# Kernel tuning notes

Hardware: AMD Instinct MI355X
Metric: run time of the kernel (lower is better)

The kernel has to match this reference:

```python
import jax, jax.numpy as jnp
import numpy as np

B = 4096
IN_DIMS = (3, 32, 32)      # in_numel = 3072
OUT_DIMS = (64, 16, 16)    # out_numel = 16384
IN_NUMEL = int(np.prod(IN_DIMS))
OUT_NUMEL = int(np.prod(OUT_DIMS))


def setup_inputs() -> dict:
    key = jax.random.key(0)
    k1, k2, k3, k4 = jax.random.split(key, 4)
    x = jax.random.normal(k1, (B,) + IN_DIMS, dtype=jnp.float32)
    # Cached composed linear operator (out_numel x in_numel); scale ~1/sqrt(fan_in)
    cached_matrix = jax.random.normal(k2, (OUT_NUMEL, IN_NUMEL), dtype=jnp.float32) / np.sqrt(IN_NUMEL)
    cached_matrix_extra = jax.random.uniform(k3, (1,), dtype=jnp.float32) + 0.5
    cached_tensor_extra = jax.random.normal(k4, (IN_NUMEL, IN_NUMEL), dtype=jnp.float32) / IN_NUMEL
    return {
        "x": x,
        "cached_matrix": cached_matrix,
        "cached_matrix_extra": cached_matrix_extra,
        "cached_tensor_extra": cached_tensor_extra,
    }


def reference(x, cached_matrix, cached_matrix_extra, cached_tensor_extra):
    batches = x.shape[0]
    # input_as_matrix: [in_numel, B]
    X = x.reshape(batches, -1).T
    # input_as_matrix_extra: L2 norm per column -> [1, B]
    X_extra = jnp.linalg.norm(X, ord=2, axis=0, keepdims=True)
    # output_as_matrix = M @ X : [out_numel, B]
    Y = jnp.matmul(cached_matrix, X)
    # output_as_matrix_extra = s * ||x|| + sum((T @ X) * X, axis=0)
    Y_extra = cached_matrix_extra * X_extra + jnp.sum(jnp.matmul(cached_tensor_extra, X) * X, axis=0, keepdims=True)
    Y = Y / Y_extra
    return Y.T.reshape(batches, *OUT_DIMS)
```

## Files before the change

kernel.cpp:

```cpp
#include <hip/hip_runtime.h>
#include <hip/hip_bf16.h>

typedef __attribute__((ext_vector_type(8))) short bf16x8;
typedef __attribute__((ext_vector_type(4))) short bf16x4;
typedef __attribute__((ext_vector_type(4))) float f32x4;

#define DEV __device__ __forceinline__

static constexpr int BATCH = 4096;
static constexpr int KDIM  = 3072;
static constexpr int NOUT  = 16384;

DEV unsigned short f2bf(float f) {
  union { float f; unsigned int u; } v; v.f = f;
  unsigned int u = v.u;
  u += 0x7fffu + ((u >> 16) & 1u);
  return (unsigned short)(u >> 16);
}

__global__ __launch_bounds__(256) void prep_x_kernel(
    const float* __restrict__ x, unsigned short* __restrict__ xbf,
    float* __restrict__ nrm) {
  const int b = blockIdx.x;
  const int t = threadIdx.x;
  const float* row = x + (size_t)b * KDIM;
  unsigned short* orow = xbf + (size_t)b * KDIM;
  float ss = 0.f;
#pragma unroll
  for (int i = 0; i < 3; ++i) {
    const int c = i * 256 + t;
    float4 v = reinterpret_cast<const float4*>(row)[c];
    ss += v.x * v.x + v.y * v.y + v.z * v.z + v.w * v.w;
    bf16x4 o;
    o[0] = (short)f2bf(v.x); o[1] = (short)f2bf(v.y);
    o[2] = (short)f2bf(v.z); o[3] = (short)f2bf(v.w);
    reinterpret_cast<bf16x4*>(orow)[c] = o;
  }
#pragma unroll
  for (int off = 32; off > 0; off >>= 1) ss += __shfl_down(ss, off, 64);
  __shared__ float red[4];
  if ((t & 63) == 0) red[t >> 6] = ss;
  __syncthreads();
  if (t == 0) nrm[b] = sqrtf(red[0] + red[1] + red[2] + red[3]);
}

__global__ __launch_bounds__(256) void cvt_kernel(
    const float* __restrict__ src, unsigned short* __restrict__ dst, size_t n4) {
  size_t i = (size_t)blockIdx.x * blockDim.x + threadIdx.x;
  const size_t stride = (size_t)gridDim.x * blockDim.x;
  for (; i < n4; i += stride) {
    float4 v = reinterpret_cast<const float4*>(src)[i];
    bf16x4 o;
    o[0] = (short)f2bf(v.x); o[1] = (short)f2bf(v.y);
    o[2] = (short)f2bf(v.z); o[3] = (short)f2bf(v.w);
    reinterpret_cast<bf16x4*>(dst)[i] = o;
  }
}

__global__ __launch_bounds__(256) void qform_kernel(
    const unsigned short* __restrict__ A,
    const unsigned short* __restrict__ Bm,
    const float* __restrict__ xf,
    float* __restrict__ partial) {
  __shared__ unsigned short ldsA[128 * 32];
  __shared__ unsigned short ldsB[128 * 32];
  const int t = threadIdx.x;
  const int lane = t & 63;
  const int wv = t >> 6;
  const int wr = wv >> 1, wc = wv & 1;
  const int col0 = blockIdx.x * 128;
  const int row0 = blockIdx.y * 128;

  f32x4 acc[4][4];
#pragma unroll
  for (int i = 0; i < 4; ++i)
#pragma unroll
    for (int j = 0; j < 4; ++j) acc[i][j] = (f32x4){0.f, 0.f, 0.f, 0.f};

  const unsigned short* aBase = A + (size_t)row0 * KDIM;
  const unsigned short* bBase = Bm + (size_t)col0 * KDIM;
  const int ldsoff0 = (t & ~63) * 8;

  for (int k0 = 0; k0 < KDIM; k0 += 32) {
    __syncthreads();
#pragma unroll
    for (int i = 0; i < 2; ++i) {
      const int c = i * 256 + t;
      const unsigned short* ga = aBase + (size_t)(c >> 2) * KDIM + (k0 + (c & 3) * 8);
      const unsigned short* gb = bBase + (size_t)(c >> 2) * KDIM + (k0 + (c & 3) * 8);
      __builtin_amdgcn_global_load_lds(
          (const __attribute__((address_space(1))) unsigned int*)(const void*)ga,
          (__attribute__((address_space(3))) unsigned int*)(void*)(ldsA + i * 2048 + ldsoff0),
          16, 0, 0);
      __builtin_amdgcn_global_load_lds(
          (const __attribute__((address_space(1))) unsigned int*)(const void*)gb,
          (__attribute__((address_space(3))) unsigned int*)(void*)(ldsB + i * 2048 + ldsoff0),
          16, 0, 0);
    }
    __syncthreads();
    bf16x8 af[4], bfr[4];
#pragma unroll
    for (int mi = 0; mi < 4; ++mi)
      af[mi] = *reinterpret_cast<const bf16x8*>(
          &ldsA[(wr * 64 + mi * 16 + (lane & 15)) * 32 + (lane >> 4) * 8]);
#pragma unroll
    for (int ni = 0; ni < 4; ++ni)
      bfr[ni] = *reinterpret_cast<const bf16x8*>(
          &ldsB[(wc * 64 + ni * 16 + (lane & 15)) * 32 + (lane >> 4) * 8]);
#pragma unroll
    for (int mi = 0; mi < 4; ++mi)
#pragma unroll
      for (int ni = 0; ni < 4; ++ni)
        acc[mi][ni] = __builtin_amdgcn_mfma_f32_16x16x32_bf16(af[mi], bfr[ni], acc[mi][ni], 0, 0, 0);
  }

#pragma unroll
  for (int mi = 0; mi < 4; ++mi) {
#pragma unroll
    for (int j = 0; j < 4; ++j) {
      const int b = row0 + wr * 64 + mi * 16 + (lane >> 4) * 4 + j;
      const float* xrow = xf + (size_t)b * KDIM + col0 + wc * 64 + (lane & 15);
      float s = 0.f;
#pragma unroll
      for (int ni = 0; ni < 4; ++ni) s += acc[mi][ni][j] * xrow[ni * 16];
      s += __shfl_xor(s, 1, 64);
      s += __shfl_xor(s, 2, 64);
      s += __shfl_xor(s, 4, 64);
      s += __shfl_xor(s, 8, 64);
      if ((lane & 15) == 0) partial[(size_t)b * 48 + blockIdx.x * 2 + wc] = s;
    }
  }
}

__global__ __launch_bounds__(256) void finalize_ye_kernel(
    const float* __restrict__ nrm, const float* __restrict__ partial,
    const float* __restrict__ sp, float* __restrict__ ye) {
  const int b = blockIdx.x * blockDim.x + threadIdx.x;
  if (b >= BATCH) return;
  float qv = 0.f;
#pragma unroll
  for (int i = 0; i < 48; ++i) qv += partial[(size_t)b * 48 + i];
  ye[b] = sp[0] * nrm[b] + qv;
}

static constexpr int BK8 = 64;

#define LDSE(BUF, OP, HALF) ((BUF)*32768 + (OP)*16384 + (HALF)*8192)

#define STAGE8(OP, HALF, S, BUF)                                             \
  {                                                                          \
    const unsigned short* gb_ = (OP) ? Bm : A;                               \
    const int gr0_ = ((OP) ? col0 : row0) + (HALF)*128;                      \
    _Pragma("unroll")                                                        \
    for (int j_ = 0; j_ < 2; ++j_) {                                         \
      const int row_ = j_*64 + wid*8 + (lane >> 3);                          \
      const int le_  = ((lane & 7)*8) ^ ((row_ & 7) << 3);                   \
      __builtin_amdgcn_global_load_lds(                                      \
        (const __attribute__((address_space(1))) unsigned int*)(const void*) \
          (gb_ + (size_t)(gr0_ + row_)*KDIM + (S)*BK8 + le_),                \
        (__attribute__((address_space(3))) unsigned int*)(void*)             \
          (lds + LDSE(BUF, OP, HALF) + j_*4096 + wid*512),                   \
        16, 0, 0);                                                           \
    }                                                                        \
  }

#define LOADA8(P, QM)                                                        \
  _Pragma("unroll")                                                          \
  for (int mi = 0; mi < 4; ++mi) {                                           \
    const int r_ = wm*64 + mi*16 + (lane & 15);                              \
    const int xv_ = (r_ & 7) << 3;                                           \
    _Pragma("unroll")                                                        \
    for (int ks = 0; ks < 2; ++ks)                                           \
      aft[mi][ks] = *reinterpret_cast<const bf16x8*>(                        \
          lds + LDSE(P, 0, QM) + ((r_*64 + ks*32 + (lane >> 4)*8) ^ xv_));   \
  }

#define LOADB8(P, QN, DST)                                                   \
  _Pragma("unroll")                                                          \
  for (int ni = 0; ni < 2; ++ni) {                                           \
    const int r_ = wn*32 + ni*16 + (lane & 15);                              \
    const int xv_ = (r_ & 7) << 3;                                           \
    _Pragma("unroll")                                                        \
    for (int ks = 0; ks < 2; ++ks)                                           \
      DST[ni][ks] = *reinterpret_cast<const bf16x8*>(                        \
          lds + LDSE(P, 1, QN) + ((r_*64 + ks*32 + (lane >> 4)*8) ^ xv_));   \
  }

#define MMA8(QM, QN, BSRC)                                                   \
  __builtin_amdgcn_s_setprio(1);                                             \
  _Pragma("unroll")                                                          \
  for (int mi = 0; mi < 4; ++mi)                                             \
    _Pragma("unroll")                                                        \
    for (int ni = 0; ni < 2; ++ni)                                           \
      _Pragma("unroll")                                                      \
      for (int ks = 0; ks < 2; ++ks)                                         \
        acc[(QM)*4 + mi][(QN)*2 + ni] =                                      \
            __builtin_amdgcn_mfma_f32_16x16x32_bf16(                         \
                aft[mi][ks], BSRC[ni][ks], acc[(QM)*4 + mi][(QN)*2 + ni],    \
                0, 0, 0);                                                    \
  __builtin_amdgcn_s_setprio(0);

#define VMW(N)                                                               \
  asm volatile("s_waitcnt vmcnt(" #N ")" ::: "memory");                      \
  __builtin_amdgcn_sched_barrier(0)

#define BARR __builtin_amdgcn_s_barrier()

#define TILE8(P, T)                                                          \
  LOADA8(P, 0); LOADB8(P, 0, bft0);                                          \
  STAGE8(1, 1, (T)+1, (P)^1);                                                \
  BARR; MMA8(0, 0, bft0); BARR;                                              \
  LOADB8(P, 1, bft1);                                                        \
  STAGE8(1, 0, (T)+1, (P)^1);                                                \
  BARR; MMA8(0, 1, bft1); BARR;                                              \
  LOADA8(P, 1);                                                              \
  STAGE8(0, 0, (T)+2, P);                                                    \
  BARR; MMA8(1, 1, bft1); BARR;                                              \
  STAGE8(0, 1, (T)+2, P);                                                    \
  BARR; MMA8(1, 0, bft0); VMW(4); BARR;

__global__ __launch_bounds__(512) void gemm8_kernel(
    const unsigned short* __restrict__ A,
    const unsigned short* __restrict__ Bm,
    const float* __restrict__ ye,
    float* __restrict__ out) {
  __shared__ unsigned short lds[65536];
  const int t = threadIdx.x;
  const int lane = t & 63, wid = t >> 6;
  const int wm = wid >> 2, wn = wid & 3;

  const int bid = blockIdx.x;
  const int wgid = (bid & 7) * 128 + (bid >> 3);
  const int bx = wgid & 63;
  const int by = wgid >> 6;
  const int row0 = by * 256, col0 = bx * 256;

  f32x4 acc[8][4];
#pragma unroll
  for (int i = 0; i < 8; ++i)
#pragma unroll
    for (int j = 0; j < 4; ++j) acc[i][j] = (f32x4){0.f, 0.f, 0.f, 0.f};

  bf16x8 aft[4][2], bft0[2][2], bft1[2][2];

  STAGE8(0, 0, 0, 0); STAGE8(1, 0, 0, 0); STAGE8(0, 1, 0, 0); STAGE8(1, 1, 0, 0);
  STAGE8(0, 0, 1, 1); STAGE8(0, 1, 1, 1);
  VMW(4);
  BARR;

#pragma unroll 1
  for (int i = 0; i < 23; ++i) {
    const int t0 = 2 * i;
    TILE8(0, t0);
    TILE8(1, t0 + 1);
  }

  LOADA8(0, 0); LOADB8(0, 0, bft0);
  STAGE8(1, 1, 47, 1);
  BARR; MMA8(0, 0, bft0); BARR;
  LOADB8(0, 1, bft1);
  STAGE8(1, 0, 47, 1);
  BARR; MMA8(0, 1, bft1); BARR;
  LOADA8(0, 1);
  BARR; MMA8(1, 1, bft1); BARR;
  MMA8(1, 0, bft0); VMW(0); BARR;
  LOADA8(1, 0); LOADB8(1, 0, bft0);
  BARR; MMA8(0, 0, bft0); BARR;
  LOADB8(1, 1, bft1);
  BARR; MMA8(0, 1, bft1); BARR;
  LOADA8(1, 1);
  BARR; MMA8(1, 1, bft1); BARR;
  MMA8(1, 0, bft0);

#pragma unroll
  for (int am = 0; am < 8; ++am) {
#pragma unroll
    for (int j = 0; j < 4; ++j) {
      const int b = row0 + (am >> 2) * 128 + wm * 64 + (am & 3) * 16 +
                    (lane >> 4) * 4 + j;
      const float r = 1.0f / ye[b];
      float* orow = out + (size_t)b * NOUT + col0;
#pragma unroll
      for (int an = 0; an < 4; ++an)
        orow[(an >> 1) * 128 + wn * 32 + (an & 1) * 16 + (lane & 15)] =
            acc[am][an][j] * r;
    }
  }
}

__global__ __launch_bounds__(256) void main_gemm_kernel(
    const unsigned short* __restrict__ A,
    const float* __restrict__ Bf,
    const float* __restrict__ ye,
    float* __restrict__ out) {
  __shared__ unsigned short ldsA[128 * 32];
  __shared__ unsigned short ldsB[128 * 32];
  const int t = threadIdx.x;
  const int lane = t & 63;
  const int wv = t >> 6;
  const int wr = wv >> 1, wc = wv & 1;
  const int col0 = blockIdx.x * 128;
  const int row0 = blockIdx.y * 128;

  f32x4 acc[4][4];
#pragma unroll
  for (int i = 0; i < 4; ++i)
#pragma unroll
    for (int j = 0; j < 4; ++j) acc[i][j] = (f32x4){0.f, 0.f, 0.f, 0.f};

  const unsigned short* aBase = A + (size_t)row0 * KDIM;
  const float* bfBase = Bf + (size_t)col0 * KDIM;
  const int ldsoff0 = (t & ~63) * 8;

  for (int k0 = 0; k0 < KDIM; k0 += 32) {
    __syncthreads();
#pragma unroll
    for (int i = 0; i < 2; ++i) {
      const int c = i * 256 + t;
      const unsigned short* ga = aBase + (size_t)(c >> 2) * KDIM + (k0 + (c & 3) * 8);
      __builtin_amdgcn_global_load_lds(
          (const __attribute__((address_space(1))) unsigned int*)(const void*)ga,
          (__attribute__((address_space(3))) unsigned int*)(void*)(ldsA + i * 2048 + ldsoff0),
          16, 0, 0);
    }
#pragma unroll
    for (int i = 0; i < 2; ++i) {
      const int c = i * 256 + t;
      const int r = c >> 1, ko = (c & 1) * 16;
      const float* gp = bfBase + (size_t)r * KDIM + k0 + ko;
      unsigned short tmp[16];
#pragma unroll
      for (int q = 0; q < 4; ++q) {
        float4 v = reinterpret_cast<const float4*>(gp)[q];
        tmp[q * 4 + 0] = f2bf(v.x); tmp[q * 4 + 1] = f2bf(v.y);
        tmp[q * 4 + 2] = f2bf(v.z); tmp[q * 4 + 3] = f2bf(v.w);
      }
#pragma unroll
      for (int q = 0; q < 2; ++q)
        *reinterpret_cast<bf16x8*>(&ldsB[r * 32 + ko + q * 8]) =
            *reinterpret_cast<const bf16x8*>(&tmp[q * 8]);
    }
    __syncthreads();
    bf16x8 af[4], bfr[4];
#pragma unroll
    for (int mi = 0; mi < 4; ++mi)
      af[mi] = *reinterpret_cast<const bf16x8*>(
          &ldsA[(wr * 64 + mi * 16 + (lane & 15)) * 32 + (lane >> 4) * 8]);
#pragma unroll
    for (int ni = 0; ni < 4; ++ni)
      bfr[ni] = *reinterpret_cast<const bf16x8*>(
          &ldsB[(wc * 64 + ni * 16 + (lane & 15)) * 32 + (lane >> 4) * 8]);
#pragma unroll
    for (int mi = 0; mi < 4; ++mi)
#pragma unroll
      for (int ni = 0; ni < 4; ++ni)
        acc[mi][ni] = __builtin_amdgcn_mfma_f32_16x16x32_bf16(af[mi], bfr[ni], acc[mi][ni], 0, 0, 0);
  }

#pragma unroll
  for (int mi = 0; mi < 4; ++mi) {
#pragma unroll
    for (int j = 0; j < 4; ++j) {
      const int b = row0 + wr * 64 + mi * 16 + (lane >> 4) * 4 + j;
      const float r = 1.0f / ye[b];
      float* orow = out + (size_t)b * NOUT + col0 + wc * 64 + (lane & 15);
#pragma unroll
      for (int ni = 0; ni < 4; ++ni) orow[ni * 16] = acc[mi][ni][j] * r;
    }
  }
}

extern "C" void kernel_launch(void* const* d_in, const int* in_sizes, int n_in,
                              void* d_out, int out_size, void* d_ws, size_t ws_size,
                              hipStream_t stream) {
  (void)in_sizes; (void)n_in; (void)out_size;
  const float* x  = (const float*)d_in[0];
  const float* M  = (const float*)d_in[1];
  const float* sc = (const float*)d_in[2];
  const float* T  = (const float*)d_in[3];
  float* out = (float*)d_out;
  char* ws = (char*)d_ws;

  size_t off = 0;
  auto wsalloc = [&](size_t bytes) -> void* {
    void* p = ws + off;
    off += (bytes + 255) & ~(size_t)255;
    return p;
  };
  unsigned short* Xbf = (unsigned short*)wsalloc((size_t)BATCH * KDIM * 2);
  unsigned short* Tbf = (unsigned short*)wsalloc((size_t)KDIM * KDIM * 2);
  float* nrm = (float*)wsalloc((size_t)BATCH * 4);
  float* ye  = (float*)wsalloc((size_t)BATCH * 4);
  float* partial = (float*)wsalloc((size_t)BATCH * 48 * 4);
  unsigned short* Mbf = (unsigned short*)wsalloc((size_t)NOUT * KDIM * 2);
  const bool useMbf = (off <= ws_size);

  prep_x_kernel<<<BATCH, 256, 0, stream>>>(x, Xbf, nrm);
  cvt_kernel<<<1024, 256, 0, stream>>>(T, Tbf, (size_t)KDIM * KDIM / 4);
  if (useMbf)
    cvt_kernel<<<2048, 256, 0, stream>>>(M, Mbf, (size_t)NOUT * KDIM / 4);
  qform_kernel<<<dim3(KDIM / 128, BATCH / 128), 256, 0, stream>>>(Xbf, Tbf, x, partial);
  finalize_ye_kernel<<<BATCH / 256, 256, 0, stream>>>(nrm, partial, sc, ye);
  if (useMbf)
    gemm8_kernel<<<dim3((NOUT / 256) * (BATCH / 256)), 512, 0, stream>>>(
        Xbf, Mbf, ye, out);
  else
    main_gemm_kernel<<<dim3(NOUT / 128, BATCH / 128), 256, 0, stream>>>(
        Xbf, M, ye, out);
}
```

Baseline: 566.8 us.

## Port quadratic-form GEMM to pipelined 256x256 split-K kernel and remap tiles

Replaces the simple 128x128 quadratic-form GEMM (T @ X, then a dot product with X) with a version of the pipelined 256x256 MFMA kernel, split four ways over K to fill the GPU. The epilogue dots the accumulators with bf16 X and reduces through LDS into the partial buffer. It also remaps the main GEMM's block-to-tile assignment per XCD and adds an lgkmcnt wait before the first MMA stage. The main risk is lower precision in the quadratic form, since it now uses bf16 X instead of fp32.

New measurement: 560.9 us. Within noise of the previous version (-1.0%).

```diff
diff --git a/kernel.cpp b/kernel.cpp
--- a/kernel.cpp
+++ b/kernel.cpp
@@ -16,6 +16,12 @@
   unsigned int u = v.u;
   u += 0x7fffu + ((u >> 16) & 1u);
   return (unsigned short)(u >> 16);
+}
+
+DEV float bf2f(unsigned short h) {
+  union { unsigned int u; float f; } v;
+  v.u = ((unsigned int)h) << 16;
+  return v.f;
 }
 
 __global__ __launch_bounds__(256) void prep_x_kernel(
@@ -54,81 +60,6 @@
     o[0] = (short)f2bf(v.x); o[1] = (short)f2bf(v.y);
     o[2] = (short)f2bf(v.z); o[3] = (short)f2bf(v.w);
     reinterpret_cast<bf16x4*>(dst)[i] = o;
-  }
-}
-
-__global__ __launch_bounds__(256) void qform_kernel(
-    const unsigned short* __restrict__ A,
-    const unsigned short* __restrict__ Bm,
-    const float* __restrict__ xf,
-    float* __restrict__ partial) {
-  __shared__ unsigned short ldsA[128 * 32];
-  __shared__ unsigned short ldsB[128 * 32];
-  const int t = threadIdx.x;
-  const int lane = t & 63;
-  const int wv = t >> 6;
-  const int wr = wv >> 1, wc = wv & 1;
-  const int col0 = blockIdx.x * 128;
-  const int row0 = blockIdx.y * 128;
-
-  f32x4 acc[4][4];
-#pragma unroll
-  for (int i = 0; i < 4; ++i)
-#pragma unroll
-    for (int j = 0; j < 4; ++j) acc[i][j] = (f32x4){0.f, 0.f, 0.f, 0.f};
-
-  const unsigned short* aBase = A + (size_t)row0 * KDIM;
-  const unsigned short* bBase = Bm + (size_t)col0 * KDIM;
-  const int ldsoff0 = (t & ~63) * 8;
-
-  for (int k0 = 0; k0 < KDIM; k0 += 32) {
-    __syncthreads();
-#pragma unroll
-    for (int i = 0; i < 2; ++i) {
-      const int c = i * 256 + t;
-      const unsigned short* ga = aBase + (size_t)(c >> 2) * KDIM + (k0 + (c & 3) * 8);
-      const unsigned short* gb = bBase + (size_t)(c >> 2) * KDIM + (k0 + (c & 3) * 8);
-      __builtin_amdgcn_global_load_lds(
-          (const __attribute__((address_space(1))) unsigned int*)(const void*)ga,
-          (__attribute__((address_space(3))) unsigned int*)(void*)(ldsA + i * 2048 + ldsoff0),
-          16, 0, 0);
-      __builtin_amdgcn_global_load_lds(
-          (const __attribute__((address_space(1))) unsigned int*)(const void*)gb,
-          (__attribute__((address_space(3))) unsigned int*)(void*)(ldsB + i * 2048 + ldsoff0),
-          16, 0, 0);
-    }
-    __syncthreads();
-    bf16x8 af[4], bfr[4];
-#pragma unroll
-    for (int mi = 0; mi < 4; ++mi)
-      af[mi] = *reinterpret_cast<const bf16x8*>(
-          &ldsA[(wr * 64 + mi * 16 + (lane & 15)) * 32 + (lane >> 4) * 8]);
-#pragma unroll
-    for (int ni = 0; ni < 4; ++ni)
-      bfr[ni] = *reinterpret_cast<const bf16x8*>(
-          &ldsB[(wc * 64 + ni * 16 + (lane & 15)) * 32 + (lane >> 4) * 8]);
-#pragma unroll
-    for (int mi = 0; mi < 4; ++mi)
-#pragma unroll
-      for (int ni = 0; ni < 4; ++ni)
-        acc[mi][ni] = __builtin_amdgcn_mfma_f32_16x16x32_bf16(af[mi], bfr[ni], acc[mi][ni], 0, 0, 0);
-  }
-
-#pragma unroll
-  for (int mi = 0; mi < 4; ++mi) {
-#pragma unroll
-    for (int j = 0; j < 4; ++j) {
-      const int b = row0 + wr * 64 + mi * 16 + (lane >> 4) * 4 + j;
-      const float* xrow = xf + (size_t)b * KDIM + col0 + wc * 64 + (lane & 15);
-      float s = 0.f;
-#pragma unroll
-      for (int ni = 0; ni < 4; ++ni) s += acc[mi][ni][j] * xrow[ni * 16];
-      s += __shfl_xor(s, 1, 64);
-      s += __shfl_xor(s, 2, 64);
-      s += __shfl_xor(s, 4, 64);
-      s += __shfl_xor(s, 8, 64);
-      if ((lane & 15) == 0) partial[(size_t)b * 48 + blockIdx.x * 2 + wc] = s;
-    }
   }
 }
 
@@ -204,11 +135,14 @@
   asm volatile("s_waitcnt vmcnt(" #N ")" ::: "memory");                      \
   __builtin_amdgcn_sched_barrier(0)
 
+#define LGKMW8 asm volatile("s_waitcnt lgkmcnt(8)" ::: "memory")
+
 #define BARR __builtin_amdgcn_s_barrier()
 
 #define TILE8(P, T)                                                          \
   LOADA8(P, 0); LOADB8(P, 0, bft0);                                          \
   STAGE8(1, 1, (T)+1, (P)^1);                                                \
+  LGKMW8;                                                                    \
   BARR; MMA8(0, 0, bft0); BARR;                                              \
   LOADB8(P, 1, bft1);                                                        \
   STAGE8(1, 0, (T)+1, (P)^1);                                                \
@@ -219,6 +153,31 @@
   STAGE8(0, 1, (T)+2, P);                                                    \
   BARR; MMA8(1, 0, bft0); VMW(4); BARR;
 
+#define PROLOG8(T0)                                                          \
+  STAGE8(0, 0, (T0), 0); STAGE8(1, 0, (T0), 0);                              \
+  STAGE8(0, 1, (T0), 0); STAGE8(1, 1, (T0), 0);                              \
+  STAGE8(0, 0, (T0)+1, 1); STAGE8(0, 1, (T0)+1, 1);                          \
+  VMW(4);                                                                    \
+  BARR;
+
+#define TAIL8(TE)                                                            \
+  LOADA8(0, 0); LOADB8(0, 0, bft0);                                          \
+  STAGE8(1, 1, (TE)+1, 1);                                                   \
+  BARR; MMA8(0, 0, bft0); BARR;                                              \
+  LOADB8(0, 1, bft1);                                                        \
+  STAGE8(1, 0, (TE)+1, 1);                                                   \
+  BARR; MMA8(0, 1, bft1); BARR;                                              \
+  LOADA8(0, 1);                                                              \
+  BARR; MMA8(1, 1, bft1); BARR;                                              \
+  MMA8(1, 0, bft0); VMW(0); BARR;                                            \
+  LOADA8(1, 0); LOADB8(1, 0, bft0);                                          \
+  BARR; MMA8(0, 0, bft0); BARR;                                              \
+  LOADB8(1, 1, bft1);                                                        \
+  BARR; MMA8(0, 1, bft1); BARR;                                              \
+  LOADA8(1, 1);                                                              \
+  BARR; MMA8(1, 1, bft1); BARR;                                              \
+  MMA8(1, 0, bft0);
+
 __global__ __launch_bounds__(512) void gemm8_kernel(
     const unsigned short* __restrict__ A,
     const unsigned short* __restrict__ Bm,
@@ -230,9 +189,9 @@
   const int wm = wid >> 2, wn = wid & 3;
 
   const int bid = blockIdx.x;
-  const int wgid = (bid & 7) * 128 + (bid >> 3);
-  const int bx = wgid & 63;
-  const int by = wgid >> 6;
+  const int xcd = bid & 7, r = bid >> 3;
+  const int by = r >> 3;
+  const int bx = xcd * 8 + (r & 7);
   const int row0 = by * 256, col0 = bx * 256;
 
   f32x4 acc[8][4];
@@ -243,34 +202,14 @@
 
   bf16x8 aft[4][2], bft0[2][2], bft1[2][2];
 
-  STAGE8(0, 0, 0, 0); STAGE8(1, 0, 0, 0); STAGE8(0, 1, 0, 0); STAGE8(1, 1, 0, 0);
-  STAGE8(0, 0, 1, 1); STAGE8(0, 1, 1, 1);
-  VMW(4);
-  BARR;
-
+  PROLOG8(0);
 #pragma unroll 1
   for (int i = 0; i < 23; ++i) {
     const int t0 = 2 * i;
     TILE8(0, t0);
     TILE8(1, t0 + 1);
   }
-
-  LOADA8(0, 0); LOADB8(0, 0, bft0);
-  STAGE8(1, 1, 47, 1);
-  BARR; MMA8(0, 0, bft0); BARR;
-  LOADB8(0, 1, bft1);
-  STAGE8(1, 0, 47, 1);
-  BARR; MMA8(0, 1, bft1); BARR;
-  LOADA8(0, 1);
-  BARR; MMA8(1, 1, bft1); BARR;
-  MMA8(1, 0, bft0); VMW(0); BARR;
-  LOADA8(1, 0); LOADB8(1, 0, bft0);
-  BARR; MMA8(0, 0, bft0); BARR;
-  LOADB8(1, 1, bft1);
-  BARR; MMA8(0, 1, bft1); BARR;
-  LOADA8(1, 1);
-  BARR; MMA8(1, 1, bft1); BARR;
-  MMA8(1, 0, bft0);
+  TAIL8(46);
 
 #pragma unroll
   for (int am = 0; am < 8; ++am) {
@@ -278,13 +217,82 @@
     for (int j = 0; j < 4; ++j) {
       const int b = row0 + (am >> 2) * 128 + wm * 64 + (am & 3) * 16 +
                     (lane >> 4) * 4 + j;
-      const float r = 1.0f / ye[b];
+      const float rr = 1.0f / ye[b];
       float* orow = out + (size_t)b * NOUT + col0;
 #pragma unroll
       for (int an = 0; an < 4; ++an)
         orow[(an >> 1) * 128 + wn * 32 + (an & 1) * 16 + (lane & 15)] =
-            acc[am][an][j] * r;
+            acc[am][an][j] * rr;
     }
+  }
+}
+
+__global__ __launch_bounds__(512) void qform8_kernel(
+    const unsigned short* __restrict__ A,
+    const unsigned short* __restrict__ Bm,
+    float* __restrict__ partial) {
+  __shared__ unsigned short lds[65536];
+  const int t = threadIdx.x;
+  const int lane = t & 63, wid = t >> 6;
+  const int wm = wid >> 2, wn = wid & 3;
+
+  const int bid = blockIdx.x;
+  const int wgid = (bid & 7) * 96 + (bid >> 3);
+  const int jt = wgid / 64;
+  const int rem = wgid % 64;
+  const int bt = rem >> 2;
+  const int ks4 = rem & 3;
+  const int row0 = bt * 256, col0 = jt * 256;
+  const int k0t = ks4 * 12;
+
+  f32x4 acc[8][4];
+#pragma unroll
+  for (int i = 0; i < 8; ++i)
+#pragma unroll
+    for (int j = 0; j < 4; ++j) acc[i][j] = (f32x4){0.f, 0.f, 0.f, 0.f};
+
+  bf16x8 aft[4][2], bft0[2][2], bft1[2][2];
+
+  PROLOG8(k0t);
+#pragma unroll 1
+  for (int i = 0; i < 5; ++i) {
+    const int t0 = k0t + 2 * i;
+    TILE8(0, t0);
+    TILE8(1, t0 + 1);
+  }
+  TAIL8(k0t + 10);
+
+  float* sred = reinterpret_cast<float*>(lds);
+#pragma unroll
+  for (int am = 0; am < 8; ++am) {
+#pragma unroll
+    for (int j = 0; j < 4; ++j) {
+      const int b = row0 + (am >> 2) * 128 + wm * 64 + (am & 3) * 16 +
+                    (lane >> 4) * 4 + j;
+      float s = 0.f;
+#pragma unroll
+      for (int an = 0; an < 4; ++an) {
+        const int col = col0 + (an >> 1) * 128 + wn * 32 + (an & 1) * 16 +
+                        (lane & 15);
+        s += acc[am][an][j] * bf2f(A[(size_t)b * KDIM + col]);
+      }
+      s += __shfl_xor(s, 1, 64);
+      s += __shfl_xor(s, 2, 64);
+      s += __shfl_xor(s, 4, 64);
+      s += __shfl_xor(s, 8, 64);
+      if ((lane & 15) == 0)
+        sred[wid * 128 + am * 16 + j * 4 + (lane >> 4)] = s;
+    }
+  }
+  __syncthreads();
+  if (t < 256) {
+    const int wmI = t >> 7, idx = t & 127;
+    const int am = idx >> 4, j = (idx >> 2) & 3, lp = idx & 3;
+    const int b = row0 + (am >> 2) * 128 + wmI * 64 + (am & 3) * 16 + lp * 4 + j;
+    float s = 0.f;
+#pragma unroll
+    for (int w2 = 0; w2 < 4; ++w2) s += sred[(wmI * 4 + w2) * 128 + idx];
+    partial[(size_t)b * 48 + jt * 4 + ks4] = s;
   }
 }
 
@@ -362,10 +370,10 @@
 #pragma unroll
     for (int j = 0; j < 4; ++j) {
       const int b = row0 + wr * 64 + mi * 16 + (lane >> 4) * 4 + j;
-      const float r = 1.0f / ye[b];
+      const float rr = 1.0f / ye[b];
       float* orow = out + (size_t)b * NOUT + col0 + wc * 64 + (lane & 15);
 #pragma unroll
-      for (int ni = 0; ni < 4; ++ni) orow[ni * 16] = acc[mi][ni][j] * r;
+      for (int ni = 0; ni < 4; ++ni) orow[ni * 16] = acc[mi][ni][j] * rr;
     }
   }
 }
@@ -399,11 +407,10 @@
   cvt_kernel<<<1024, 256, 0, stream>>>(T, Tbf, (size_t)KDIM * KDIM / 4);
   if (useMbf)
     cvt_kernel<<<2048, 256, 0, stream>>>(M, Mbf, (size_t)NOUT * KDIM / 4);
-  qform_kernel<<<dim3(KDIM / 128, BATCH / 128), 256, 0, stream>>>(Xbf, Tbf, x, partial);
+  qform8_kernel<<<768, 512, 0, stream>>>(Xbf, Tbf, partial);
   finalize_ye_kernel<<<BATCH / 256, 256, 0, stream>>>(nrm, partial, sc, ye);
   if (useMbf)
-    gemm8_kernel<<<dim3((NOUT / 256) * (BATCH / 256)), 512, 0, stream>>>(
-        Xbf, Mbf, ye, out);
+    gemm8_kernel<<<1024, 512, 0, stream>>>(Xbf, Mbf, ye, out);
   else
     main_gemm_kernel<<<dim3(NOUT / 128, BATCH / 128), 256, 0, stream>>>(
         Xbf, M, ye, out);
```
